# Kernel optimization log

Hardware: AMD Instinct MI355X
Metric: run time of the kernel (lower is better)

## Reference

```python
import jax, jax.numpy as jnp
import numpy as np

N = 50000      # nodes in batched graph
E = 800000     # directed edges
F_IN = 64      # node_feature_dim
F_E = 16       # edge_feature_dim
H = 4          # heads
C = 64         # hidden_dim per head
HC = H * C     # 256


def setup_inputs() -> dict:
    key = jax.random.key(0)
    ks = jax.random.split(key, 26)
    rn = lambda k, s, scale=0.1: jax.random.normal(k, s, dtype=jnp.float32) * scale
    inp = {}
    inp["x"] = rn(ks[0], (N, F_IN), 1.0)
    inp["edge_src"] = jax.random.randint(ks[1], (E,), 0, N)
    inp["edge_dst"] = jax.random.randint(ks[2], (E,), 0, N)
    inp["edge_attr"] = rn(ks[3], (E, F_E), 1.0)
    # GATConv layer 1 params
    inp["W1"] = rn(ks[4], (F_IN, HC))
    inp["atts1"] = rn(ks[5], (H, C))
    inp["attd1"] = rn(ks[6], (H, C))
    inp["We1"] = rn(ks[7], (F_E, HC))
    inp["atte1"] = rn(ks[8], (H, C))
    inp["b1"] = jnp.zeros((HC,), jnp.float32)
    inp["g1"] = jnp.ones((HC,), jnp.float32)
    inp["be1"] = jnp.zeros((HC,), jnp.float32)
    # GATConv layer 2 params
    inp["W2"] = rn(ks[9], (HC, HC))
    inp["atts2"] = rn(ks[10], (H, C))
    inp["attd2"] = rn(ks[11], (H, C))
    inp["We2"] = rn(ks[12], (F_E, HC))
    inp["atte2"] = rn(ks[13], (H, C))
    inp["b2"] = jnp.zeros((HC,), jnp.float32)
    inp["g2"] = jnp.ones((HC,), jnp.float32)
    inp["be2"] = jnp.zeros((HC,), jnp.float32)
    # output head
    inp["Wout"] = rn(ks[14], (HC, 1))
    inp["bout"] = jnp.zeros((1,), jnp.float32)
    return inp


def _gat_layer(x, src, dst, eattr, W, att_s, att_d, We, att_e, b):
    """PyG GATConv (concat=True, add_self_loops with fill_value='mean', eval so no dropout)."""
    n = x.shape[0]
    e = src.shape[0]
    # self-loop edge attr = mean of incoming edge attrs per node (0 if none)
    deg = jax.ops.segment_sum(jnp.ones((e,), x.dtype), dst, num_segments=n)
    loop_attr = jax.ops.segment_sum(eattr, dst, num_segments=n) / jnp.maximum(deg, 1.0)[:, None]
    loop = jnp.arange(n)
    src2 = jnp.concatenate([src, loop])
    dst2 = jnp.concatenate([dst, loop])
    ea2 = jnp.concatenate([eattr, loop_attr], axis=0)
    xs = (x @ W).reshape(n, H, C)                          # [N,H,C]
    a_s = jnp.einsum('nhc,hc->nh', xs, att_s)              # [N,H]
    a_d = jnp.einsum('nhc,hc->nh', xs, att_d)
    ee = (ea2 @ We).reshape(-1, H, C)                      # [E+N,H,C]
    a_e = jnp.einsum('ehc,hc->eh', ee, att_e)
    logits = jax.nn.leaky_relu(a_s[src2] + a_d[dst2] + a_e, 0.2)  # [E+N,H]
    m = jax.ops.segment_max(logits, dst2, num_segments=n)
    p = jnp.exp(logits - m[dst2])
    denom = jax.ops.segment_sum(p, dst2, num_segments=n)[dst2] + 1e-16
    alpha = p / denom                                      # segment softmax per dst node
    out = jax.ops.segment_sum(xs[src2] * alpha[:, :, None], dst2, num_segments=n)
    return out.reshape(n, HC) + b


def _bn_relu(x, g, b):
    # BatchNorm1d in training mode (batch statistics), eps=1e-5
    mu = x.mean(axis=0)
    var = ((x - mu) ** 2).mean(axis=0)
    return jax.nn.relu(g * (x - mu) * jax.lax.rsqrt(var + 1e-5) + b)


def reference(x, edge_src, edge_dst, edge_attr,
              W1, atts1, attd1, We1, atte1, b1, g1, be1,
              W2, atts2, attd2, We2, atte2, b2, g2, be2,
              Wout, bout):
    h = _gat_layer(x, edge_src, edge_dst, edge_attr, W1, atts1, attd1, We1, atte1, b1)
    h = _bn_relu(h, g1, be1)
    h = _gat_layer(h, edge_src, edge_dst, edge_attr, W2, atts2, attd2, We2, atte2, b2)
    h = _bn_relu(h, g2, be2)
    return h @ Wout + bout
```

## Files before the change

### kernel.cpp

```cpp
#include <hip/hip_runtime.h>
#include <hip/hip_bf16.h>
#include <stdint.h>

#define NNODES 50000
#define NEDGES 800000
#define HC 256

typedef unsigned short u16;
typedef __attribute__((ext_vector_type(8))) short bf16x8;
typedef __attribute__((ext_vector_type(4))) float f32x4;

__device__ __forceinline__ float b2f(u16 v) {
    return __uint_as_float(((unsigned)v) << 16);
}
__device__ __forceinline__ u16 f2b(float f) {
    unsigned u = __float_as_uint(f);
    u += 0x7fff + ((u >> 16) & 1);
    return (u16)(u >> 16);
}

__device__ __constant__ int dPO[19] = {0,16384,16640,16896,20992,21248,21504,21760,22016,
                                       87552,87808,88064,92160,92416,92672,92928,93184,93440,93441};
static const int hPO[19] = {0,16384,16640,16896,20992,21248,21504,21760,22016,
                            87552,87808,88064,92160,92416,92672,92928,93184,93440,93441};
#define TOTP 93441

__global__ void zero_init(unsigned* __restrict__ p, long nwords) {
    long i = (long)blockIdx.x * blockDim.x + threadIdx.x;
    long stride = (long)gridDim.x * blockDim.x;
    for (; i < nwords; i += stride) p[i] = 0u;
}

__global__ void detect_dtype(const unsigned* __restrict__ xbits, int* __restrict__ flag) {
    __shared__ int cnt;
    if (threadIdx.x == 0) cnt = 0;
    __syncthreads();
    int sane = 0;
    for (int i = threadIdx.x; i < 1024; i += 256) {
        unsigned lo = xbits[i] & 0xffffu;
        int e = (int)((lo >> 7) & 0xff);
        if (e >= 117 && e <= 133) sane++;
    }
    atomicAdd(&cnt, sane);
    __syncthreads();
    if (threadIdx.x == 0) *flag = (cnt >= 512) ? 1 : 0;
}

__global__ void cvt_bf16(const void* __restrict__ src, u16* __restrict__ dst, int n,
                         const int* __restrict__ flag) {
    int isbf16 = *flag;
    int i = blockIdx.x * 256 + threadIdx.x;
    int stride = gridDim.x * 256;
    if (isbf16) {
        const u16* s = (const u16*)src;
        for (; i < n; i += stride) dst[i] = s[i];
    } else {
        const float* s = (const float*)src;
        for (; i < n; i += stride) dst[i] = f2b(s[i]);
    }
}

struct Ptrs18 { const void* s[18]; };
__global__ void cvt_params(Ptrs18 p, u16* __restrict__ dst, const int* __restrict__ flag) {
    int i = blockIdx.x * 256 + threadIdx.x;
    if (i >= TOTP) return;
    int isbf16 = *flag;
    int idx = 0;
    #pragma unroll
    for (int j = 1; j < 18; j++) idx += (i >= dPO[j]) ? 1 : 0;
    int rel = i - dPO[idx];
    dst[i] = isbf16 ? ((const u16*)p.s[idx])[rel] : f2b(((const float*)p.s[idx])[rel]);
}

__global__ void proj_weight(const u16* __restrict__ W, const u16* __restrict__ att,
                            float* __restrict__ out, int R) {
    int i = blockIdx.x * 256 + threadIdx.x;
    if (i >= R * 4) return;
    int f = i >> 2, h = i & 3;
    float s = 0.f;
    for (int c = 0; c < 64; c++)
        s += b2f(W[f * 256 + h * 64 + c]) * b2f(att[h * 64 + c]);
    out[i] = s;
}

__global__ void proj_weight2(const u16* __restrict__ W, const u16* __restrict__ atta,
                             const u16* __restrict__ attb,
                             float* __restrict__ outa, float* __restrict__ outb, int R) {
    int i = blockIdx.x * 256 + threadIdx.x;
    if (i >= R * 4) return;
    int f = i >> 2, h = i & 3;
    float sa = 0.f, sb = 0.f;
    for (int c = 0; c < 64; c++) {
        float w = b2f(W[f * 256 + h * 64 + c]);
        sa += w * b2f(atta[h * 64 + c]);
        sb += w * b2f(attb[h * 64 + c]);
    }
    outa[i] = sa;
    outb[i] = sb;
}

__global__ void transpose_w(const u16* __restrict__ W, u16* __restrict__ WT, int K) {
    int i = blockIdx.x * 256 + threadIdx.x;
    if (i >= K * 256) return;
    int k = i / 256, c = i % 256;
    WT[c * K + k] = W[i];
}

__global__ void edge_deg(const int* __restrict__ edst, int* __restrict__ deg) {
    int e = blockIdx.x * 256 + threadIdx.x;
    if (e >= NEDGES) return;
    atomicAdd(&deg[edst[e]], 1);
}

__global__ void block_sum(const int* __restrict__ deg, int* __restrict__ bsums, int n) {
    __shared__ int lds[256];
    int i = blockIdx.x * 256 + threadIdx.x;
    lds[threadIdx.x] = (i < n) ? deg[i] : 0;
    __syncthreads();
    for (int s = 128; s; s >>= 1) {
        if (threadIdx.x < s) lds[threadIdx.x] += lds[threadIdx.x + s];
        __syncthreads();
    }
    if (threadIdx.x == 0) bsums[blockIdx.x] = lds[0];
}

__global__ void scan_bsums(const int* __restrict__ bsums, int* __restrict__ boffs, int nb) {
    __shared__ int lds[256];
    int t = threadIdx.x;
    int v = (t < nb) ? bsums[t] : 0;
    lds[t] = v;
    __syncthreads();
    for (int s = 1; s < 256; s <<= 1) {
        int u = (t >= s) ? lds[t - s] : 0;
        __syncthreads();
        lds[t] += u;
        __syncthreads();
    }
    boffs[t] = lds[t] - v;
}

__global__ void write_offsets(const int* __restrict__ deg, const int* __restrict__ boffs,
                              int* __restrict__ off, int* __restrict__ cursor, int n) {
    __shared__ int lds[256];
    int t = threadIdx.x;
    int i = blockIdx.x * 256 + t;
    int v = (i < n) ? deg[i] : 0;
    lds[t] = v;
    __syncthreads();
    for (int s = 1; s < 256; s <<= 1) {
        int u = (t >= s) ? lds[t - s] : 0;
        __syncthreads();
        lds[t] += u;
        __syncthreads();
    }
    int exc = lds[t] - v + boffs[blockIdx.x];
    if (i < n) { off[i] = exc; cursor[i] = exc; }
}

__global__ __launch_bounds__(256) void edge_stage(
    const void* __restrict__ eattr_raw, const int* __restrict__ flag,
    const int* __restrict__ esrc, const int* __restrict__ edst,
    const float* __restrict__ ve1, const float* __restrict__ ve2,
    int* __restrict__ cursor, uint4* __restrict__ rec) {
    int e = blockIdx.x * 256 + threadIdx.x;
    if (e >= NEDGES) return;
    float a[16];
    if (*flag) {
        const u16* s = (const u16*)eattr_raw + (long)e * 16;
        const uint4* q = (const uint4*)s;
        uint4 q0 = q[0], q1 = q[1];
        unsigned w0[8] = {q0.x, q0.y, q0.z, q0.w, q1.x, q1.y, q1.z, q1.w};
        #pragma unroll
        for (int j = 0; j < 8; j++) {
            a[2 * j] = b2f((u16)(w0[j] & 0xffff));
            a[2 * j + 1] = b2f((u16)(w0[j] >> 16));
        }
    } else {
        const float* s = (const float*)eattr_raw + (long)e * 16;
        #pragma unroll
        for (int j = 0; j < 16; j += 4) {
            float4 q = *(const float4*)(s + j);
            a[j] = q.x; a[j + 1] = q.y; a[j + 2] = q.z; a[j + 3] = q.w;
        }
    }
    float s1[4], s2[4];
    #pragma unroll
    for (int h = 0; h < 4; h++) {
        float t1 = 0.f, t2 = 0.f;
        #pragma unroll
        for (int f = 0; f < 16; f++) {
            t1 += a[f] * ve1[f * 4 + h];
            t2 += a[f] * ve2[f * 4 + h];
        }
        s1[h] = t1;
        s2[h] = t2;
    }
    unsigned a1lo = (unsigned)f2b(s1[0]) | ((unsigned)f2b(s1[1]) << 16);
    unsigned a1hi = (unsigned)f2b(s1[2]) | ((unsigned)f2b(s1[3]) << 16);
    unsigned a2lo = (unsigned)f2b(s2[0]) | ((unsigned)f2b(s2[1]) << 16);
    unsigned a2hi = (unsigned)f2b(s2[2]) | ((unsigned)f2b(s2[3]) << 16);
    int d = edst[e];
    int p = atomicAdd(&cursor[d], 1);
    unsigned src = (unsigned)esrc[e];
    rec[(long)p * 2 + 0] = make_uint4(src, a1lo, a1hi, 0u);
    rec[(long)p * 2 + 1] = make_uint4(src, a2lo, a2hi, 0u);
}

template <int K>
__global__ __launch_bounds__(256) void gemm_mfma(const u16* __restrict__ A,
                                                 const u16* __restrict__ WT,
                                                 u16* __restrict__ out) {
    int tid = threadIdx.x;
    int wave = tid >> 6, lane = tid & 63;
    int quad = lane >> 4, l15 = lane & 15;
    long row0 = (long)blockIdx.x * 16;
    const u16* Arow = A + (row0 + l15) * K + quad * 8;
    const u16* Wbase = WT + (long)(wave * 64 + l15) * K + quad * 8;
    f32x4 acc[4] = {};
    for (int kk = 0; kk < K; kk += 32) {
        bf16x8 av = *(const bf16x8*)(Arow + kk);
        #pragma unroll
        for (int nt = 0; nt < 4; nt++) {
            bf16x8 bv = *(const bf16x8*)(Wbase + (long)nt * 16 * K + kk);
            acc[nt] = __builtin_amdgcn_mfma_f32_16x16x32_bf16(av, bv, acc[nt], 0, 0, 0);
        }
    }
    u16* orow = out + row0 * HC;
    #pragma unroll
    for (int nt = 0; nt < 4; nt++) {
        #pragma unroll
        for (int j = 0; j < 4; j++) {
            int r = quad * 4 + j;
            int c = wave * 64 + nt * 16 + l15;
            orow[(long)r * HC + c] = f2b(acc[nt][j]);
        }
    }
}

template <int K>
__global__ __launch_bounds__(256) void proj_att(const u16* __restrict__ X,
                                                const float* __restrict__ us,
                                                const float* __restrict__ ud,
                                                float* __restrict__ as_, float* __restrict__ ad_) {
    int wid = (blockIdx.x * 256 + threadIdx.x) >> 6;
    int lane = threadIdx.x & 63;
    if (wid >= NNODES) return;
    float pas[4] = {0.f, 0.f, 0.f, 0.f}, pad[4] = {0.f, 0.f, 0.f, 0.f};
    const u16* row = X + (long)wid * K;
    for (int f = lane; f < K; f += 64) {
        float xv = b2f(row[f]);
        #pragma unroll
        for (int h = 0; h < 4; h++) {
            pas[h] += xv * us[f * 4 + h];
            pad[h] += xv * ud[f * 4 + h];
        }
    }
    #pragma unroll
    for (int h = 0; h < 4; h++) {
        for (int o = 32; o; o >>= 1) {
            pas[h] += __shfl_down(pas[h], o);
            pad[h] += __shfl_down(pad[h], o);
        }
    }
    if (lane == 0) {
        #pragma unroll
        for (int h = 0; h < 4; h++) {
            as_[wid * 4 + h] = pas[h];
            ad_[wid * 4 + h] = pad[h];
        }
    }
}

__global__ __launch_bounds__(256) void gat_fused(
    const u16* __restrict__ xs, const float* __restrict__ as_, const float* __restrict__ ad_,
    const uint4* __restrict__ rec, int layer,
    const int* __restrict__ off, const int* __restrict__ deg,
    const u16* __restrict__ bias, u16* __restrict__ out) {
    __shared__ int s_lds[4][64];
    __shared__ float w_lds[4][64][4];
    int wid = (blockIdx.x * 256 + threadIdx.x) >> 6;
    if (wid >= NNODES) return;
    int wave = threadIdx.x >> 6;
    int lane = threadIdx.x & 63;
    int d = wid;
    int st = off[d], dg = deg[d];
    int slot = lane >> 2, h = lane & 3;
    float adv = ad_[d * 4 + h];
    float m = -1e30f, s = 0.f, sae = 0.f;

    if (dg <= 64) {
        for (int i = slot; i < dg; i += 16) {
            uint4 r4 = rec[(long)(st + i) * 2 + layer];
            int src = (int)r4.x;
            unsigned wsel = (h & 2) ? r4.z : r4.y;
            float aev = b2f((u16)((h & 1) ? (wsel >> 16) : (wsel & 0xffffu)));
            float t = as_[src * 4 + h] + adv + aev;
            float lg = (t > 0.f) ? t : 0.2f * t;
            if (h == 0) s_lds[wave][i] = src;
            w_lds[wave][i][h] = lg;
            sae += aev;
            float mn = fmaxf(m, lg);
            s = s * __expf(m - mn) + __expf(lg - mn);
            m = mn;
        }
        #pragma unroll
        for (int o = 4; o < 64; o <<= 1) {
            float mo = __shfl_xor(m, o), so = __shfl_xor(s, o), ao = __shfl_xor(sae, o);
            float mn = fmaxf(m, mo);
            s = s * __expf(m - mn) + so * __expf(mo - mn);
            m = mn;
            sae += ao;
        }
        float invs, wself;
        {
            float asv = as_[d * 4 + h];
            float l0 = asv + adv + sae / fmaxf((float)dg, 1.f);
            l0 = (l0 > 0.f) ? l0 : 0.2f * l0;
            float mn = fmaxf(m, l0);
            s = s * __expf(m - mn) + __expf(l0 - mn);
            m = mn;
            invs = 1.f / s;
            wself = __expf(l0 - mn) * invs;
        }
        for (int i = slot; i < dg; i += 16)
            w_lds[wave][i][h] = __expf(w_lds[wave][i][h] - m) * invs;

        int cg = lane & 31, half = lane >> 5;
        int ch8 = cg * 8;
        int h2 = cg >> 3;
        float ws2 = __shfl(wself, h2);
        const u16* xbase = xs + ch8;
        float a0, a1, a2, a3, a4, a5, a6, a7;
        {
            uint4 v = *(const uint4*)(xbase + (long)d * HC);
            float wsf = half ? 0.f : ws2;
            a0 = wsf * b2f((u16)(v.x & 0xffffu)); a1 = wsf * b2f((u16)(v.x >> 16));
            a2 = wsf * b2f((u16)(v.y & 0xffffu)); a3 = wsf * b2f((u16)(v.y >> 16));
            a4 = wsf * b2f((u16)(v.z & 0xffffu)); a5 = wsf * b2f((u16)(v.z >> 16));
            a6 = wsf * b2f((u16)(v.w & 0xffffu)); a7 = wsf * b2f((u16)(v.w >> 16));
        }
        int i = half;
        for (; i + 2 < dg; i += 4) {
            float wA = w_lds[wave][i][h2];     int sA = s_lds[wave][i];
            float wB = w_lds[wave][i + 2][h2]; int sB = s_lds[wave][i + 2];
            uint4 vA = *(const uint4*)(xbase + (long)sA * HC);
            uint4 vB = *(const uint4*)(xbase + (long)sB * HC);
            a0 += wA * b2f((u16)(vA.x & 0xffffu)) + wB * b2f((u16)(vB.x & 0xffffu));
            a1 += wA * b2f((u16)(vA.x >> 16))     + wB * b2f((u16)(vB.x >> 16));
            a2 += wA * b2f((u16)(vA.y & 0xffffu)) + wB * b2f((u16)(vB.y & 0xffffu));
            a3 += wA * b2f((u16)(vA.y >> 16))     + wB * b2f((u16)(vB.y >> 16));
            a4 += wA * b2f((u16)(vA.z & 0xffffu)) + wB * b2f((u16)(vB.z & 0xffffu));
            a5 += wA * b2f((u16)(vA.z >> 16))     + wB * b2f((u16)(vB.z >> 16));
            a6 += wA * b2f((u16)(vA.w & 0xffffu)) + wB * b2f((u16)(vB.w & 0xffffu));
            a7 += wA * b2f((u16)(vA.w >> 16))     + wB * b2f((u16)(vB.w >> 16));
        }
        for (; i < dg; i += 2) {
            float wA = w_lds[wave][i][h2]; int sA = s_lds[wave][i];
            uint4 vA = *(const uint4*)(xbase + (long)sA * HC);
            a0 += wA * b2f((u16)(vA.x & 0xffffu)); a1 += wA * b2f((u16)(vA.x >> 16));
            a2 += wA * b2f((u16)(vA.y & 0xffffu)); a3 += wA * b2f((u16)(vA.y >> 16));
            a4 += wA * b2f((u16)(vA.z & 0xffffu)); a5 += wA * b2f((u16)(vA.z >> 16));
            a6 += wA * b2f((u16)(vA.w & 0xffffu)); a7 += wA * b2f((u16)(vA.w >> 16));
        }
        a0 += __shfl_xor(a0, 32); a1 += __shfl_xor(a1, 32);
        a2 += __shfl_xor(a2, 32); a3 += __shfl_xor(a3, 32);
        a4 += __shfl_xor(a4, 32); a5 += __shfl_xor(a5, 32);
        a6 += __shfl_xor(a6, 32); a7 += __shfl_xor(a7, 32);
        if (half == 0) {
            uint4 bv = *(const uint4*)(bias + ch8);
            a0 += b2f((u16)(bv.x & 0xffffu)); a1 += b2f((u16)(bv.x >> 16));
            a2 += b2f((u16)(bv.y & 0xffffu)); a3 += b2f((u16)(bv.y >> 16));
            a4 += b2f((u16)(bv.z & 0xffffu)); a5 += b2f((u16)(bv.z >> 16));
            a6 += b2f((u16)(bv.w & 0xffffu)); a7 += b2f((u16)(bv.w >> 16));
            uint4 ov;
            ov.x = (unsigned)f2b(a0) | ((unsigned)f2b(a1) << 16);
            ov.y = (unsigned)f2b(a2) | ((unsigned)f2b(a3) << 16);
            ov.z = (unsigned)f2b(a4) | ((unsigned)f2b(a5) << 16);
            ov.w = (unsigned)f2b(a6) | ((unsigned)f2b(a7) << 16);
            *(uint4*)(out + (long)d * HC + ch8) = ov;
        }
        return;
    }

    for (int base = 0; base < dg; base += 16) {
        int i = base + slot;
        float lg = -1e30f, aev = 0.f, w = 0.f;
        if (i < dg) {
            uint4 r4 = rec[(long)(st + i) * 2 + layer];
            int src = (int)r4.x;
            unsigned wsel = (h & 2) ? r4.z : r4.y;
            aev = b2f((u16)((h & 1) ? (wsel >> 16) : (wsel & 0xffffu)));
            float t = as_[src * 4 + h] + adv + aev;
            lg = (t > 0.f) ? t : 0.2f * t;
        }
        sae += aev;
        float mn = fmaxf(m, lg);
        if (i < dg) w = __expf(lg - mn);
        s = s * __expf(m - mn) + w;
        m = mn;
    }
    #pragma unroll
    for (int o = 4; o < 64; o <<= 1) {
        float mo = __shfl_xor(m, o), so = __shfl_xor(s, o), ao = __shfl_xor(sae, o);
        float mn = fmaxf(m, mo);
        s = s * __expf(m - mn) + so * __expf(mo - mn);
        m = mn;
        sae += ao;
    }
    float invs, wself;
    {
        float asv = as_[d * 4 + h];
        float l0 = asv + adv + sae / fmaxf((float)dg, 1.f);
        l0 = (l0 > 0.f) ? l0 : 0.2f * l0;
        float mn = fmaxf(m, l0);
        s = s * __expf(m - mn) + __expf(l0 - mn);
        m = mn;
        invs = 1.f / s;
        wself = __expf(l0 - mn) * invs;
    }
    int h2 = lane >> 4;
    float m2 = __shfl(m, h2);
    float is2 = __shfl(invs, h2);
    float ws2 = __shfl(wself, h2);
    float adv2 = __shfl(adv, h2);
    int cb = lane * 4;
    float a0, a1, a2, a3;
    {
        uint2 v = *(const uint2*)(xs + (long)d * HC + cb);
        a0 = ws2 * b2f((u16)(v.x & 0xffffu)); a1 = ws2 * b2f((u16)(v.x >> 16));
        a2 = ws2 * b2f((u16)(v.y & 0xffffu)); a3 = ws2 * b2f((u16)(v.y >> 16));
    }
    int slot16 = lane & 15;
    int lhi = lane & 48;
    for (int base = 0; base < dg; base += 16) {
        int cnt = min(16, dg - base);
        float wv = 0.f;
        int srcl = 0;
        if (slot16 < cnt) {
            uint4 r4 = rec[(long)(st + base + slot16) * 2 + layer];
            srcl = (int)r4.x;
            unsigned wsel = (h2 & 2) ? r4.z : r4.y;
            float aev = b2f((u16)((h2 & 1) ? (wsel >> 16) : (wsel & 0xffffu)));
            float t = as_[srcl * 4 + h2] + adv2 + aev;
            t = (t > 0.f) ? t : 0.2f * t;
            wv = __expf(t - m2) * is2;
        }
        for (int j = 0; j < cnt; j++) {
            float w0 = __shfl(wv, lhi | j);
            int s0 = __shfl(srcl, j);
            uint2 v0 = *(const uint2*)(xs + (long)s0 * HC + cb);
            a0 += w0 * b2f((u16)(v0.x & 0xffffu));
            a1 += w0 * b2f((u16)(v0.x >> 16));
            a2 += w0 * b2f((u16)(v0.y & 0xffffu));
            a3 += w0 * b2f((u16)(v0.y >> 16));
        }
    }
    u16 o0 = f2b(a0 + b2f(bias[cb + 0]));
    u16 o1 = f2b(a1 + b2f(bias[cb + 1]));
    u16 o2 = f2b(a2 + b2f(bias[cb + 2]));
    u16 o3 = f2b(a3 + b2f(bias[cb + 3]));
    uint2 ov;
    ov.x = (unsigned)o0 | ((unsigned)o1 << 16);
    ov.y = (unsigned)o2 | ((unsigned)o3 << 16);
    *(uint2*)(out + (long)d * HC + cb) = ov;
}

__global__ void bn_stats(const u16* __restrict__ h, float* __restrict__ stats) {
    int c = threadIdx.x;
    float s = 0.f, q = 0.f;
    for (int r = blockIdx.x; r < NNODES; r += gridDim.x) {
        float v = b2f(h[(long)r * HC + c]);
        s += v;
        q += v * v;
    }
    atomicAdd(&stats[c], s);
    atomicAdd(&stats[256 + c], q);
}

__global__ void bn_apply(u16* __restrict__ h, const float* __restrict__ stats,
                         const u16* __restrict__ g, const u16* __restrict__ be) {
    long i = (long)blockIdx.x * 256 + threadIdx.x;
    if (i >= (long)NNODES * HC) return;
    int c = (int)(i & 255);
    float mu = stats[c] * (1.0f / NNODES);
    float var = stats[256 + c] * (1.0f / NNODES) - mu * mu;
    var = fmaxf(var, 0.f);
    float rs = rsqrtf(var + 1e-5f);
    float v = b2f(h[i]);
    float y = b2f(g[c]) * (v - mu) * rs + b2f(be[c]);
    h[i] = f2b(fmaxf(y, 0.f));
}

__global__ __launch_bounds__(256) void out_head(const u16* __restrict__ h,
                                                const u16* __restrict__ wout,
                                                const u16* __restrict__ bout,
                                                void* __restrict__ y,
                                                const int* __restrict__ flag) {
    int wid = (blockIdx.x * 256 + threadIdx.x) >> 6;
    int lane = threadIdx.x & 63;
    if (wid >= NNODES) return;
    const u16* r = h + (long)wid * HC + lane * 4;
    float p = b2f(r[0]) * b2f(wout[lane * 4 + 0]) + b2f(r[1]) * b2f(wout[lane * 4 + 1]) +
              b2f(r[2]) * b2f(wout[lane * 4 + 2]) + b2f(r[3]) * b2f(wout[lane * 4 + 3]);
    for (int o = 32; o; o >>= 1) p += __shfl_down(p, o);
    if (lane == 0) {
        float v = p + b2f(bout[0]);
        if (*flag) ((u16*)y)[wid] = f2b(v);
        else       ((float*)y)[wid] = v;
    }
}

extern "C" void kernel_launch(void* const* d_in, const int* in_sizes, int n_in,
                              void* d_out, int out_size, void* d_ws, size_t ws_size,
                              hipStream_t stream) {
    (void)in_sizes; (void)n_in; (void)out_size; (void)ws_size;
    const void* x_raw     = d_in[0];
    const int*  esrc      = (const int*)d_in[1];
    const int*  edst      = (const int*)d_in[2];
    const void* eattr_raw = d_in[3];

    char* ws = (char*)d_ws;
    size_t o = 0;
    auto alloc = [&](size_t bytes) -> char* {
        o = (o + 255) & ~(size_t)255;
        char* p = ws + o;
        o += bytes;
        return p;
    };
    int* dflag = (int*)alloc(256);
    u16* xb   = (u16*)alloc((size_t)NNODES * 64 * 2);
    u16* pall = (u16*)alloc((size_t)TOTP * 2);
    u16 *W1b = pall + hPO[0], *atts1b = pall + hPO[1], *attd1b = pall + hPO[2],
        *We1b = pall + hPO[3], *atte1b = pall + hPO[4], *b1b = pall + hPO[5],
        *g1b = pall + hPO[6], *be1b = pall + hPO[7], *W2b = pall + hPO[8],
        *atts2b = pall + hPO[9], *attd2b = pall + hPO[10], *We2b = pall + hPO[11],
        *atte2b = pall + hPO[12], *b2b = pall + hPO[13], *g2b = pall + hPO[14],
        *be2b = pall + hPO[15], *Woutb = pall + hPO[16], *boutb = pall + hPO[17];
    u16* WT1 = (u16*)alloc(256 * 64 * 2);
    u16* WT2 = (u16*)alloc(256 * 256 * 2);
    float* ve1 = (float*)alloc(64 * 4);
    float* ve2 = (float*)alloc(64 * 4);
    float* us1 = (float*)alloc(256 * 4);
    float* ud1 = (float*)alloc(256 * 4);
    float* us2 = (float*)alloc(1024 * 4);
    float* ud2 = (float*)alloc(1024 * 4);
    int* deg = (int*)alloc((size_t)NNODES * 4);
    float* stats1 = (float*)alloc(512 * 4);
    float* stats2 = (float*)alloc(512 * 4);
    size_t zero_end = o;
    size_t zero_begin = (size_t)((char*)deg - ws);
    int* off = (int*)alloc((size_t)NNODES * 4);
    int* cursor = (int*)alloc((size_t)NNODES * 4);
    int* bsums = (int*)alloc(256 * 4);
    int* boffs = (int*)alloc(256 * 4);
    uint4* rec = (uint4*)alloc((size_t)NEDGES * 32);
    float* as_ = (float*)alloc((size_t)NNODES * 16);
    float* ad_ = (float*)alloc((size_t)NNODES * 16);
    u16* bufA = (u16*)alloc((size_t)NNODES * HC * 2);
    u16* bufB = (u16*)alloc((size_t)NNODES * HC * 2);

    long zwords = (long)((zero_end - zero_begin) / 4);
    zero_init<<<128, 256, 0, stream>>>((unsigned*)(ws + zero_begin), zwords);
    detect_dtype<<<1, 256, 0, stream>>>((const unsigned*)x_raw, dflag);

    cvt_bf16<<<2048, 256, 0, stream>>>(x_raw, xb, NNODES * 64, dflag);
    Ptrs18 pp;
    for (int i = 0; i < 18; i++) pp.s[i] = d_in[4 + i];
    cvt_params<<<(TOTP + 255) / 256, 256, 0, stream>>>(pp, pall, dflag);

    transpose_w<<<64, 256, 0, stream>>>(W1b, WT1, 64);
    transpose_w<<<256, 256, 0, stream>>>(W2b, WT2, 256);
    proj_weight<<<1, 256, 0, stream>>>(We1b, atte1b, ve1, 16);
    proj_weight<<<1, 256, 0, stream>>>(We2b, atte2b, ve2, 16);
    proj_weight2<<<1, 256, 0, stream>>>(W1b, atts1b, attd1b, us1, ud1, 64);
    proj_weight2<<<4, 256, 0, stream>>>(W2b, atts2b, attd2b, us2, ud2, 256);

    int eblocks = (NEDGES + 255) / 256;
    int nb = (NNODES + 255) / 256;
    edge_deg<<<eblocks, 256, 0, stream>>>(edst, deg);
    block_sum<<<nb, 256, 0, stream>>>(deg, bsums, NNODES);
    scan_bsums<<<1, 256, 0, stream>>>(bsums, boffs, nb);
    write_offsets<<<nb, 256, 0, stream>>>(deg, boffs, off, cursor, NNODES);
    edge_stage<<<eblocks, 256, 0, stream>>>(eattr_raw, dflag, esrc, edst, ve1, ve2,
                                            cursor, rec);

    int mtiles = NNODES / 16;
    int wblocks = (NNODES * 64 + 255) / 256;

    gemm_mfma<64><<<mtiles, 256, 0, stream>>>(xb, WT1, bufA);
    proj_att<64><<<wblocks, 256, 0, stream>>>(xb, us1, ud1, as_, ad_);
    gat_fused<<<wblocks, 256, 0, stream>>>(bufA, as_, ad_, rec, 0, off, deg, b1b, bufB);
    bn_stats<<<512, 256, 0, stream>>>(bufB, stats1);
    bn_apply<<<(NNODES * HC + 255) / 256, 256, 0, stream>>>(bufB, stats1, g1b, be1b);

    gemm_mfma<256><<<mtiles, 256, 0, stream>>>(bufB, WT2, bufA);
    proj_att<256><<<wblocks, 256, 0, stream>>>(bufB, us2, ud2, as_, ad_);
    gat_fused<<<wblocks, 256, 0, stream>>>(bufA, as_, ad_, rec, 1, off, deg, b2b, bufB);
    bn_stats<<<512, 256, 0, stream>>>(bufB, stats2);
    bn_apply<<<(NNODES * HC + 255) / 256, 256, 0, stream>>>(bufB, stats2, g2b, be2b);

    out_head<<<wblocks, 256, 0, stream>>>(bufB, Woutb, boutb, d_out, dflag);
}
```

Before: 624.0 us.

## Fold BatchNorm+ReLU into consumer kernels and unroll aggregation gather loop

Drops the standalone bn_apply passes. A tiny bn_coef kernel now computes per-channel scale and shift, and the BN+ReLU transform is applied on the fly inside the layer-2 GEMM, proj_att and out_head as they load activations. This removes two full read-modify-write passes over the 50000x256 bf16 feature buffer, at the cost of extra ALU work and coefficient loads inside the consumers. The neighbor gather loop in gat_fused is also unrolled from 2 to 4 rows per iteration to keep more loads in flight.

```diff
diff --git a/kernel.cpp b/kernel.cpp
--- a/kernel.cpp
+++ b/kernel.cpp
@@ -206,9 +206,22 @@
     rec[(long)p * 2 + 1] = make_uint4(src, a2lo, a2hi, 0u);
 }
 
-template <int K>
+__global__ void bn_coef(const float* __restrict__ stats, const u16* __restrict__ g,
+                        const u16* __restrict__ be, float* __restrict__ coef) {
+    int c = threadIdx.x;
+    float mu = stats[c] * (1.0f / NNODES);
+    float var = stats[256 + c] * (1.0f / NNODES) - mu * mu;
+    var = fmaxf(var, 0.f);
+    float rs = rsqrtf(var + 1e-5f);
+    float sc = b2f(g[c]) * rs;
+    coef[c] = sc;
+    coef[256 + c] = b2f(be[c]) - sc * mu;
+}
+
+template <int K, bool BN>
 __global__ __launch_bounds__(256) void gemm_mfma(const u16* __restrict__ A,
                                                  const u16* __restrict__ WT,
+                                                 const float* __restrict__ coef,
                                                  u16* __restrict__ out) {
     int tid = threadIdx.x;
     int wave = tid >> 6, lane = tid & 63;
@@ -219,6 +232,21 @@
     f32x4 acc[4] = {};
     for (int kk = 0; kk < K; kk += 32) {
         bf16x8 av = *(const bf16x8*)(Arow + kk);
+        if (BN) {
+            int kb = kk + quad * 8;
+            float4 sc0 = *(const float4*)(coef + kb);
+            float4 sc1 = *(const float4*)(coef + kb + 4);
+            float4 sh0 = *(const float4*)(coef + 256 + kb);
+            float4 sh1 = *(const float4*)(coef + 256 + kb + 4);
+            float scl[8] = {sc0.x, sc0.y, sc0.z, sc0.w, sc1.x, sc1.y, sc1.z, sc1.w};
+            float shf[8] = {sh0.x, sh0.y, sh0.z, sh0.w, sh1.x, sh1.y, sh1.z, sh1.w};
+            #pragma unroll
+            for (int j = 0; j < 8; j++) {
+                float v = b2f((u16)av[j]);
+                v = fmaxf(v * scl[j] + shf[j], 0.f);
+                av[j] = (short)f2b(v);
+            }
+        }
         #pragma unroll
         for (int nt = 0; nt < 4; nt++) {
             bf16x8 bv = *(const bf16x8*)(Wbase + (long)nt * 16 * K + kk);
@@ -237,8 +265,9 @@
     }
 }
 
-template <int K>
+template <int K, bool BN>
 __global__ __launch_bounds__(256) void proj_att(const u16* __restrict__ X,
+                                                const float* __restrict__ coef,
                                                 const float* __restrict__ us,
                                                 const float* __restrict__ ud,
                                                 float* __restrict__ as_, float* __restrict__ ad_) {
@@ -249,6 +278,7 @@
     const u16* row = X + (long)wid * K;
     for (int f = lane; f < K; f += 64) {
         float xv = b2f(row[f]);
+        if (BN) xv = fmaxf(xv * coef[f] + coef[256 + f], 0.f);
         #pragma unroll
         for (int h = 0; h < 4; h++) {
             pas[h] += xv * us[f * 4 + h];
@@ -287,10 +317,11 @@
     int slot = lane >> 2, h = lane & 3;
     float adv = ad_[d * 4 + h];
     float m = -1e30f, s = 0.f, sae = 0.f;
+    const uint4* rbase = rec + (long)st * 2 + layer;
 
     if (dg <= 64) {
         for (int i = slot; i < dg; i += 16) {
-            uint4 r4 = rec[(long)(st + i) * 2 + layer];
+            uint4 r4 = rbase[(long)i * 2];
             int src = (int)r4.x;
             unsigned wsel = (h & 2) ? r4.z : r4.y;
             float aev = b2f((u16)((h & 1) ? (wsel >> 16) : (wsel & 0xffffu)));
@@ -340,19 +371,31 @@
             a6 = wsf * b2f((u16)(v.w & 0xffffu)); a7 = wsf * b2f((u16)(v.w >> 16));
         }
         int i = half;
-        for (; i + 2 < dg; i += 4) {
+        for (; i + 6 < dg; i += 8) {
             float wA = w_lds[wave][i][h2];     int sA = s_lds[wave][i];
             float wB = w_lds[wave][i + 2][h2]; int sB = s_lds[wave][i + 2];
+            float wC = w_lds[wave][i + 4][h2]; int sC = s_lds[wave][i + 4];
+            float wD = w_lds[wave][i + 6][h2]; int sD = s_lds[wave][i + 6];
             uint4 vA = *(const uint4*)(xbase + (long)sA * HC);
             uint4 vB = *(const uint4*)(xbase + (long)sB * HC);
-            a0 += wA * b2f((u16)(vA.x & 0xffffu)) + wB * b2f((u16)(vB.x & 0xffffu));
-            a1 += wA * b2f((u16)(vA.x >> 16))     + wB * b2f((u16)(vB.x >> 16));
-            a2 += wA * b2f((u16)(vA.y & 0xffffu)) + wB * b2f((u16)(vB.y & 0xffffu));
-            a3 += wA * b2f((u16)(vA.y >> 16))     + wB * b2f((u16)(vB.y >> 16));
-            a4 += wA * b2f((u16)(vA.z & 0xffffu)) + wB * b2f((u16)(vB.z & 0xffffu));
-            a5 += wA * b2f((u16)(vA.z >> 16))     + wB * b2f((u16)(vB.z >> 16));
-            a6 += wA * b2f((u16)(vA.w & 0xffffu)) + wB * b2f((u16)(vB.w & 0xffffu));
-            a7 += wA * b2f((u16)(vA.w >> 16))     + wB * b2f((u16)(vB.w >> 16));
+            uint4 vC = *(const uint4*)(xbase + (long)sC * HC);
+            uint4 vD = *(const uint4*)(xbase + (long)sD * HC);
+            a0 += wA * b2f((u16)(vA.x & 0xffffu)) + wB * b2f((u16)(vB.x & 0xffffu))
+                + wC * b2f((u16)(vC.x & 0xffffu)) + wD * b2f((u16)(vD.x & 0xffffu));
+            a1 += wA * b2f((u16)(vA.x >> 16))     + wB * b2f((u16)(vB.x >> 16))
+                + wC * b2f((u16)(vC.x >> 16))     + wD * b2f((u16)(vD.x >> 16));
+            a2 += wA * b2f((u16)(vA.y & 0xffffu)) + wB * b2f((u16)(vB.y & 0xffffu))
+                + wC * b2f((u16)(vC.y & 0xffffu)) + wD * b2f((u16)(vD.y & 0xffffu));
+            a3 += wA * b2f((u16)(vA.y >> 16))     + wB * b2f((u16)(vB.y >> 16))
+                + wC * b2f((u16)(vC.y >> 16))     + wD * b2f((u16)(vD.y >> 16));
+            a4 += wA * b2f((u16)(vA.z & 0xffffu)) + wB * b2f((u16)(vB.z & 0xffffu))
+                + wC * b2f((u16)(vC.z & 0xffffu)) + wD * b2f((u16)(vD.z & 0xffffu));
+            a5 += wA * b2f((u16)(vA.z >> 16))     + wB * b2f((u16)(vB.z >> 16))
+                + wC * b2f((u16)(vC.z >> 16))     + wD * b2f((u16)(vD.z >> 16));
+            a6 += wA * b2f((u16)(vA.w & 0xffffu)) + wB * b2f((u16)(vB.w & 0xffffu))
+                + wC * b2f((u16)(vC.w & 0xffffu)) + wD * b2f((u16)(vD.w & 0xffffu));
+            a7 += wA * b2f((u16)(vA.w >> 16))     + wB * b2f((u16)(vB.w >> 16))
+                + wC * b2f((u16)(vC.w >> 16))     + wD * b2f((u16)(vD.w >> 16));
         }
         for (; i < dg; i += 2) {
             float wA = w_lds[wave][i][h2]; int sA = s_lds[wave][i];
@@ -386,7 +429,7 @@
         int i = base + slot;
         float lg = -1e30f, aev = 0.f, w = 0.f;
         if (i < dg) {
-            uint4 r4 = rec[(long)(st + i) * 2 + layer];
+            uint4 r4 = rbase[(long)i * 2];
             int src = (int)r4.x;
             unsigned wsel = (h & 2) ? r4.z : r4.y;
             aev = b2f((u16)((h & 1) ? (wsel >> 16) : (wsel & 0xffffu)));
@@ -437,7 +480,7 @@
         float wv = 0.f;
         int srcl = 0;
         if (slot16 < cnt) {
-            uint4 r4 = rec[(long)(st + base + slot16) * 2 + layer];
+            uint4 r4 = rbase[(long)(base + slot16) * 2];
             srcl = (int)r4.x;
             unsigned wsel = (h2 & 2) ? r4.z : r4.y;
             float aev = b2f((u16)((h2 & 1) ? (wsel >> 16) : (wsel & 0xffffu)));
@@ -477,21 +520,8 @@
     atomicAdd(&stats[256 + c], q);
 }
 
-__global__ void bn_apply(u16* __restrict__ h, const float* __restrict__ stats,
-                         const u16* __restrict__ g, const u16* __restrict__ be) {
-    long i = (long)blockIdx.x * 256 + threadIdx.x;
-    if (i >= (long)NNODES * HC) return;
-    int c = (int)(i & 255);
-    float mu = stats[c] * (1.0f / NNODES);
-    float var = stats[256 + c] * (1.0f / NNODES) - mu * mu;
-    var = fmaxf(var, 0.f);
-    float rs = rsqrtf(var + 1e-5f);
-    float v = b2f(h[i]);
-    float y = b2f(g[c]) * (v - mu) * rs + b2f(be[c]);
-    h[i] = f2b(fmaxf(y, 0.f));
-}
-
 __global__ __launch_bounds__(256) void out_head(const u16* __restrict__ h,
+                                                const float* __restrict__ coef,
                                                 const u16* __restrict__ wout,
                                                 const u16* __restrict__ bout,
                                                 void* __restrict__ y,
@@ -500,8 +530,14 @@
     int lane = threadIdx.x & 63;
     if (wid >= NNODES) return;
     const u16* r = h + (long)wid * HC + lane * 4;
-    float p = b2f(r[0]) * b2f(wout[lane * 4 + 0]) + b2f(r[1]) * b2f(wout[lane * 4 + 1]) +
-              b2f(r[2]) * b2f(wout[lane * 4 + 2]) + b2f(r[3]) * b2f(wout[lane * 4 + 3]);
+    int c0 = lane * 4;
+    float p = 0.f;
+    #pragma unroll
+    for (int j = 0; j < 4; j++) {
+        float v = b2f(r[j]);
+        v = fmaxf(v * coef[c0 + j] + coef[256 + c0 + j], 0.f);
+        p += v * b2f(wout[c0 + j]);
+    }
     for (int o = 32; o; o >>= 1) p += __shfl_down(p, o);
     if (lane == 0) {
         float v = p + b2f(bout[0]);
@@ -544,6 +580,8 @@
     float* ud1 = (float*)alloc(256 * 4);
     float* us2 = (float*)alloc(1024 * 4);
     float* ud2 = (float*)alloc(1024 * 4);
+    float* coef1 = (float*)alloc(512 * 4);
+    float* coef2 = (float*)alloc(512 * 4);
     int* deg = (int*)alloc((size_t)NNODES * 4);
     float* stats1 = (float*)alloc(512 * 4);
     float* stats2 = (float*)alloc(512 * 4);
@@ -587,17 +625,17 @@
     int mtiles = NNODES / 16;
     int wblocks = (NNODES * 64 + 255) / 256;
 
-    gemm_mfma<64><<<mtiles, 256, 0, stream>>>(xb, WT1, bufA);
-    proj_att<64><<<wblocks, 256, 0, stream>>>(xb, us1, ud1, as_, ad_);
+    gemm_mfma<64, false><<<mtiles, 256, 0, stream>>>(xb, WT1, nullptr, bufA);
+    proj_att<64, false><<<wblocks, 256, 0, stream>>>(xb, nullptr, us1, ud1, as_, ad_);
     gat_fused<<<wblocks, 256, 0, stream>>>(bufA, as_, ad_, rec, 0, off, deg, b1b, bufB);
     bn_stats<<<512, 256, 0, stream>>>(bufB, stats1);
-    bn_apply<<<(NNODES * HC + 255) / 256, 256, 0, stream>>>(bufB, stats1, g1b, be1b);
-
-    gemm_mfma<256><<<mtiles, 256, 0, stream>>>(bufB, WT2, bufA);
-    proj_att<256><<<wblocks, 256, 0, stream>>>(bufB, us2, ud2, as_, ad_);
+    bn_coef<<<1, 256, 0, stream>>>(stats1, g1b, be1b, coef1);
+
+    gemm_mfma<256, true><<<mtiles, 256, 0, stream>>>(bufB, WT2, coef1, bufA);
+    proj_att<256, true><<<wblocks, 256, 0, stream>>>(bufB, coef1, us2, ud2, as_, ad_);
     gat_fused<<<wblocks, 256, 0, stream>>>(bufA, as_, ad_, rec, 1, off, deg, b2b, bufB);
     bn_stats<<<512, 256, 0, stream>>>(bufB, stats2);
-    bn_apply<<<(NNODES * HC + 255) / 256, 256, 0, stream>>>(bufB, stats2, g2b, be2b);
-
-    out_head<<<wblocks, 256, 0, stream>>>(bufB, Woutb, boutb, d_out, dflag);
-}
+    bn_coef<<<1, 256, 0, stream>>>(stats2, g2b, be2b, coef2);
+
+    out_head<<<wblocks, 256, 0, stream>>>(bufB, coef2, Woutb, boutb, d_out, dflag);
+}
```

After: 621.1 us. Within noise of the previous version (-0.5%).
